# Kernel tuning notes

Measured on AMD Instinct MI355X. Metric: run time of the kernel, lower is better.

The kernel has to match this reference:

```python
import jax, jax.numpy as jnp
import numpy as np

N, E, D, L = 50000, 800000, 128, 4


def setup_inputs() -> dict:
    key = jax.random.key(0)
    k0, k1, k2, k3 = jax.random.split(key, 4)
    x = jax.random.normal(k0, (N, D), dtype=jnp.float32)
    edge_index = jax.random.randint(k1, (2, E), 0, N, dtype=jnp.int32)
    # per-layer GCNConv weights [L, D, D] and biases [L, D]
    W = jax.random.normal(k2, (L, D, D), dtype=jnp.float32) * (1.0 / np.sqrt(D))
    b = jax.random.normal(k3, (L, D), dtype=jnp.float32) * 0.01
    batch_index = jnp.zeros((N,), dtype=jnp.int32)
    node_rankings = jnp.zeros((N,), dtype=jnp.int32)
    return {"x": x, "edge_index": edge_index, "batch_index": batch_index,
            "node_rankings": node_rankings, "W": W, "b": b}


def reference(x, edge_index, batch_index, node_rankings, W, b):
    # NullControl contributes 0; dropout_rate=0 / eval -> identity.
    n = x.shape[0]
    loops = jnp.arange(n, dtype=edge_index.dtype)
    row = jnp.concatenate([edge_index[0], loops])  # sources (with self-loops)
    col = jnp.concatenate([edge_index[1], loops])  # destinations
    # symmetric GCN normalization: deg over destinations, norm = d_i^-1/2 d_j^-1/2
    deg = jax.ops.segment_sum(jnp.ones_like(row, dtype=x.dtype), col, num_segments=n)
    dinv = jnp.where(deg > 0, jax.lax.rsqrt(deg), 0.0)
    norm = dinv[row] * dinv[col]  # [E+N]
    for l in range(W.shape[0]):
        h = x @ W[l]                      # [N, D] dense transform
        msg = h[row] * norm[:, None]      # [E+N, D] gathered, scaled messages
        agg = jax.ops.segment_sum(msg, col, num_segments=n)  # scatter-add
        x = jax.nn.relu(agg + b[l])       # control(=0) + bias + relu
    return x
```

## Files before the change

kernel.cpp:

```cpp
#include <hip/hip_runtime.h>

#define D 128
#define NLAYERS 4

typedef unsigned short ushort_t;
typedef unsigned int uint_t;
typedef __attribute__((ext_vector_type(8))) short short8;
typedef __attribute__((ext_vector_type(4))) float f32x4;

__device__ __forceinline__ ushort_t f2bf(float f) {
    uint_t u = __float_as_uint(f);
    u += 0x7FFFu + ((u >> 16) & 1u);
    return (ushort_t)(u >> 16);
}
__device__ __forceinline__ float bf_lo(uint_t u) {
    return __uint_as_float(u << 16);
}
__device__ __forceinline__ float bf_hi(uint_t u) {
    return __uint_as_float(u & 0xFFFF0000u);
}
__device__ __forceinline__ uint_t pack2(float a, float b) {
    return (uint_t)f2bf(a) | ((uint_t)f2bf(b) << 16);
}


__global__ void k_count_deg(const int* __restrict__ dsts, int E,
                            int* __restrict__ deg, int* __restrict__ slot) {
    int i = blockIdx.x * blockDim.x + threadIdx.x;
    if (i < E) slot[i] = atomicAdd(&deg[dsts[i]], 1);
}

__global__ void k_scan1(const int* __restrict__ deg, int n, int* __restrict__ prow,
                        int* __restrict__ partials, float* __restrict__ dinv) {
    __shared__ int wsum[4];
    int tid = threadIdx.x;
    int base = blockIdx.x * 1024 + tid * 4;
    int g0 = (base + 0 < n) ? deg[base + 0] : -8;
    int g1 = (base + 1 < n) ? deg[base + 1] : -8;
    int g2 = (base + 2 < n) ? deg[base + 2] : -8;
    int g3 = (base + 3 < n) ? deg[base + 3] : -8;
    if (base + 0 < n) dinv[base + 0] = rsqrtf((float)(g0 + 1));
    if (base + 1 < n) dinv[base + 1] = rsqrtf((float)(g1 + 1));
    if (base + 2 < n) dinv[base + 2] = rsqrtf((float)(g2 + 1));
    if (base + 3 < n) dinv[base + 3] = rsqrtf((float)(g3 + 1));
    int p0 = (g0 + 8) & ~7;
    int p1 = (g1 + 8) & ~7;
    int p2 = (g2 + 8) & ~7;
    int p3 = (g3 + 8) & ~7;
    int s = p0 + p1 + p2 + p3;
    int lane = tid & 63;
    int incl = s;
    #pragma unroll
    for (int off = 1; off < 64; off <<= 1) {
        int y = __shfl_up(incl, off);
        if (lane >= off) incl += y;
    }
    int wid = tid >> 6;
    if (lane == 63) wsum[wid] = incl;
    __syncthreads();
    int wprev = 0;
    for (int w = 0; w < wid; w++) wprev += wsum[w];
    int excl = wprev + (incl - s);
    if (base + 0 < n) prow[base + 0] = excl;
    if (base + 1 < n) prow[base + 1] = excl + p0;
    if (base + 2 < n) prow[base + 2] = excl + p0 + p1;
    if (base + 3 < n) prow[base + 3] = excl + p0 + p1 + p2;
    if (tid == 255) partials[blockIdx.x] = wprev + incl;
}

__global__ void k_scan23(int* __restrict__ prow, const int* __restrict__ partials,
                         int n, int nb) {
    int i = blockIdx.x * blockDim.x + threadIdx.x;
    int chunk = (blockIdx.x * blockDim.x) >> 10;
    int pre = 0;
    for (int j = 0; j < chunk; j++) pre += partials[j];
    if (i < n) prow[i] += pre;
    if (i == 0) {
        int tot = 0;
        for (int j = 0; j < nb; j++) tot += partials[j];
        prow[n] = tot;
    }
}

__global__ void k_prep(const int* __restrict__ srcs, const int* __restrict__ dsts,
                       const int* __restrict__ deg, const int* __restrict__ slot,
                       const int* __restrict__ prow, const float* __restrict__ dinv,
                       const float* __restrict__ x, const float* __restrict__ W,
                       int* __restrict__ ewi, ushort_t* __restrict__ xs0,
                       ushort_t* __restrict__ xs1, ushort_t* __restrict__ Wt_hi,
                       ushort_t* __restrict__ Wt_lo, int n, int E,
                       int B1, int B2, int B3, int B4) {
    int b = blockIdx.x;
    int tid = threadIdx.x;
    if (b < B1) {
        int i = b * 256 + tid;
        if (i < E) {
            int c = dsts[i];
            ewi[prow[c] + 1 + slot[i]] = srcs[i];
        }
    } else if (b < B2) {
        int i = (b - B1) * 256 + tid;
        if (i < n) {
            int base = prow[i];
            int len = deg[i] + 1;
            int plen = (deg[i] + 8) & ~7;
            ewi[base] = i;
            for (int j = len; j < plen; j++) ewi[base + j] = n;
        }
    } else if (b < B3) {
        int idx = (b - B2) * 256 + tid;
        if (idx < n * (D / 4)) {
            int row = idx >> 5;
            float di = dinv[row];
            float4 v = ((const float4*)x)[idx];
            uint2 o;
            o.x = pack2(di * v.x, di * v.y);
            o.y = pack2(di * v.z, di * v.w);
            ((uint2*)xs0)[idx] = o;
        }
    } else if (b < B4) {
        int t = (b - B3) * 256 + tid;
        int l = t >> 14;
        int k = (t >> 7) & 127;
        int nn = t & 127;
        float w = W[((size_t)l << 14) + k * 128 + nn];
        ushort_t hi = f2bf(w);
        float wf = __uint_as_float((uint_t)hi << 16);
        ushort_t lo = f2bf(w - wf);
        size_t o = ((size_t)l << 14) + nn * 128 + k;
        Wt_hi[o] = hi;
        Wt_lo[o] = lo;
    } else {
        if (tid < 128) xs0[(size_t)n * D + tid] = 0;
        else xs1[(size_t)n * D + (tid - 128)] = 0;
    }
}

__global__ __launch_bounds__(256) void k_aggregate(
    const ushort_t* __restrict__ xs, const int* __restrict__ prow,
    const int* __restrict__ ewi, const float* __restrict__ dinv,
    ushort_t* __restrict__ s, int n) {
    int node = (blockIdx.x * 256 + threadIdx.x) >> 5;
    if (node >= n) return;
    int lane = threadIdx.x & 63;
    int sub = (lane >> 4) & 1;
    int t = lane & 15;
    float di = dinv[node];

    float acc[8] = {0.f, 0.f, 0.f, 0.f, 0.f, 0.f, 0.f, 0.f};
    int e = prow[node], end = prow[node + 1];
    for (; e < end; e += 8) {
        int4 gg = *(const int4*)(ewi + e + sub * 4);
        uint4 v0 = *(const uint4*)(xs + (size_t)gg.x * D + t * 8);
        uint4 v1 = *(const uint4*)(xs + (size_t)gg.y * D + t * 8);
        uint4 v2 = *(const uint4*)(xs + (size_t)gg.z * D + t * 8);
        uint4 v3 = *(const uint4*)(xs + (size_t)gg.w * D + t * 8);
        acc[0] += bf_lo(v0.x); acc[1] += bf_hi(v0.x);
        acc[2] += bf_lo(v0.y); acc[3] += bf_hi(v0.y);
        acc[4] += bf_lo(v0.z); acc[5] += bf_hi(v0.z);
        acc[6] += bf_lo(v0.w); acc[7] += bf_hi(v0.w);
        acc[0] += bf_lo(v1.x); acc[1] += bf_hi(v1.x);
        acc[2] += bf_lo(v1.y); acc[3] += bf_hi(v1.y);
        acc[4] += bf_lo(v1.z); acc[5] += bf_hi(v1.z);
        acc[6] += bf_lo(v1.w); acc[7] += bf_hi(v1.w);
        acc[0] += bf_lo(v2.x); acc[1] += bf_hi(v2.x);
        acc[2] += bf_lo(v2.y); acc[3] += bf_hi(v2.y);
        acc[4] += bf_lo(v2.z); acc[5] += bf_hi(v2.z);
        acc[6] += bf_lo(v2.w); acc[7] += bf_hi(v2.w);
        acc[0] += bf_lo(v3.x); acc[1] += bf_hi(v3.x);
        acc[2] += bf_lo(v3.y); acc[3] += bf_hi(v3.y);
        acc[4] += bf_lo(v3.z); acc[5] += bf_hi(v3.z);
        acc[6] += bf_lo(v3.w); acc[7] += bf_hi(v3.w);
    }
    #pragma unroll
    for (int q = 0; q < 8; q++) acc[q] += __shfl_xor(acc[q], 16);
    if (sub == 0) {
        ushort_t* dst = s + (size_t)node * D + t * 8;
        uint4 o;
        o.x = pack2(di * acc[0], di * acc[1]);
        o.y = pack2(di * acc[2], di * acc[3]);
        o.z = pack2(di * acc[4], di * acc[5]);
        o.w = pack2(di * acc[6], di * acc[7]);
        *(uint4*)dst = o;
    }
}

__global__ __launch_bounds__(256) void k_gemm_mfma(
    const ushort_t* __restrict__ A, const ushort_t* __restrict__ Wt_hi,
    const ushort_t* __restrict__ Wt_lo, const float* __restrict__ bias,
    const float* __restrict__ dinv, float* __restrict__ out_f32,
    ushort_t* __restrict__ out_bf, int n) {
    int tid = threadIdx.x;
    int wave = tid >> 6;
    int lane = tid & 63;
    int lg = lane >> 4;
    int lr = lane & 15;
    int base_row = blockIdx.x * 128 + wave * 32;

    short8 a[2][4];
    #pragma unroll
    for (int st = 0; st < 2; st++) {
        int r = base_row + st * 16 + lr;
        if (r > n - 1) r = n - 1;
        const ushort_t* ap = A + (size_t)r * D + lg * 8;
        #pragma unroll
        for (int k0 = 0; k0 < 4; k0++)
            a[st][k0] = *(const short8*)(ap + k0 * 32);
    }

    f32x4 acc[2][8];
    #pragma unroll
    for (int st = 0; st < 2; st++)
        #pragma unroll
        for (int nt = 0; nt < 8; nt++)
            acc[st][nt] = (f32x4){0.f, 0.f, 0.f, 0.f};

    #pragma unroll
    for (int nt = 0; nt < 8; nt++) {
        const ushort_t* wh = Wt_hi + (size_t)(nt * 16 + lr) * D + lg * 8;
        const ushort_t* wl = Wt_lo + (size_t)(nt * 16 + lr) * D + lg * 8;
        #pragma unroll
        for (int k0 = 0; k0 < 4; k0++) {
            short8 bh = *(const short8*)(wh + k0 * 32);
            short8 bl = *(const short8*)(wl + k0 * 32);
            acc[0][nt] = __builtin_amdgcn_mfma_f32_16x16x32_bf16(a[0][k0], bh, acc[0][nt], 0, 0, 0);
            acc[0][nt] = __builtin_amdgcn_mfma_f32_16x16x32_bf16(a[0][k0], bl, acc[0][nt], 0, 0, 0);
            acc[1][nt] = __builtin_amdgcn_mfma_f32_16x16x32_bf16(a[1][k0], bh, acc[1][nt], 0, 0, 0);
            acc[1][nt] = __builtin_amdgcn_mfma_f32_16x16x32_bf16(a[1][k0], bl, acc[1][nt], 0, 0, 0);
        }
    }

    #pragma unroll
    for (int nt = 0; nt < 8; nt++) {
        int col = nt * 16 + lr;
        float bv = bias[col];
        #pragma unroll
        for (int st = 0; st < 2; st++) {
            #pragma unroll
            for (int r = 0; r < 4; r++) {
                int grow = base_row + st * 16 + lg * 4 + r;
                float o = fmaxf(acc[st][nt][r] + bv, 0.f);
                float op = __shfl_xor(o, 1);
                if ((lr & 1) == 0 && grow < n) {
                    if (out_bf) {
                        float dsc = dinv[grow];
                        *(uint_t*)(out_bf + (size_t)grow * D + col) = pack2(dsc * o, dsc * op);
                    } else {
                        float2 ov; ov.x = o; ov.y = op;
                        *(float2*)(out_f32 + (size_t)grow * D + col) = ov;
                    }
                }
            }
        }
    }
}


extern "C" void kernel_launch(void* const* d_in, const int* in_sizes, int n_in,
                              void* d_out, int out_size, void* d_ws, size_t ws_size,
                              hipStream_t stream) {
    const float* x   = (const float*)d_in[0];
    const int* eidx  = (const int*)d_in[1];
    const float* W   = (const float*)d_in[4];
    const float* b   = (const float*)d_in[5];
    float* out       = (float*)d_out;

    const int N = in_sizes[0] / D;
    const int E = in_sizes[1] / 2;
    const int* srcs = eidx;
    const int* dsts = eidx + E;

    char* ws = (char*)d_ws;
    size_t off = 0;
    auto alloc = [&](size_t bytes) -> void* {
        void* p = ws + off;
        off = (off + bytes + 511) & ~(size_t)511;
        return p;
    };
    int*      deg      = (int*)alloc((size_t)N * 4);
    float*    dinv     = (float*)alloc((size_t)N * 4);
    int*      prow     = (int*)alloc((size_t)(N + 1) * 4);
    int*      partials = (int*)alloc(256 * 4);
    int*      ewi      = (int*)alloc((size_t)(E + 8 * N) * 4);
    ushort_t* s_buf    = (ushort_t*)alloc((size_t)N * D * 2);
    ushort_t* xh0      = (ushort_t*)alloc(((size_t)N + 1) * D * 2);
    ushort_t* xh1      = (ushort_t*)alloc(((size_t)N + 1) * D * 2);
    ushort_t* wt_hi    = (ushort_t*)alloc((size_t)NLAYERS * D * D * 2);
    ushort_t* wt_lo    = (ushort_t*)alloc((size_t)NLAYERS * D * D * 2);
    int*      slot     = (int*)s_buf;
    (void)ws_size; (void)n_in; (void)out_size;

    hipMemsetAsync(deg, 0, (size_t)N * 4, stream);

    int tE = (E + 255) / 256;
    int tN = (N + 255) / 256;
    int nbScan = (N + 1023) / 1024;

    k_count_deg<<<tE, 256, 0, stream>>>(dsts, E, deg, slot);
    k_scan1<<<nbScan, 256, 0, stream>>>(deg, N, prow, partials, dinv);
    k_scan23<<<tN, 256, 0, stream>>>(prow, partials, N, nbScan);

    int B1 = tE;
    int B2 = B1 + tN;
    int B3 = B2 + (N * (D / 4) + 255) / 256;
    int B4 = B3 + (NLAYERS * D * D) / 256;
    k_prep<<<B4 + 1, 256, 0, stream>>>(srcs, dsts, deg, slot, prow, dinv, x, W,
                                       ewi, xh0, xh1, wt_hi, wt_lo, N, E,
                                       B1, B2, B3, B4);

    int aggBlocks = (N + 7) / 8;
    int gemmBlocks = (N + 127) / 128;

    const ushort_t* xin = xh0;
    for (int l = 0; l < NLAYERS; l++) {
        k_aggregate<<<aggBlocks, 256, 0, stream>>>(xin, prow, ewi, dinv, s_buf, N);
        bool last = (l == NLAYERS - 1);
        ushort_t* xout = last ? nullptr : ((l & 1) ? xh0 : xh1);
        k_gemm_mfma<<<gemmBlocks, 256, 0, stream>>>(
            s_buf, wt_hi + (size_t)l * D * D, wt_lo + (size_t)l * D * D,
            b + (size_t)l * D, dinv, last ? out : nullptr, xout, N);
        xin = xout;
    }
}
```

Before: 372.8 us.

## Split bf16 feature matrices into 16-column panels for cache-local aggregation

```diff
diff --git a/kernel.cpp b/kernel.cpp
--- a/kernel.cpp
+++ b/kernel.cpp
@@ -2,6 +2,8 @@
 
 #define D 128
 #define NLAYERS 4
+#define NPANEL 8
+#define PCOLS 16
 
 typedef unsigned short ushort_t;
 typedef unsigned int uint_t;
@@ -90,6 +92,7 @@
                        ushort_t* __restrict__ xs1, ushort_t* __restrict__ Wt_hi,
                        ushort_t* __restrict__ Wt_lo, int n, int E,
                        int B1, int B2, int B3, int B4) {
+    const size_t PS = (size_t)(n + 1) * PCOLS;
     int b = blockIdx.x;
     int tid = threadIdx.x;
     if (b < B1) {
@@ -111,12 +114,13 @@
         int idx = (b - B2) * 256 + tid;
         if (idx < n * (D / 4)) {
             int row = idx >> 5;
+            int col0 = (idx & 31) * 4;
             float di = dinv[row];
             float4 v = ((const float4*)x)[idx];
             uint2 o;
             o.x = pack2(di * v.x, di * v.y);
             o.y = pack2(di * v.z, di * v.w);
-            ((uint2*)xs0)[idx] = o;
+            *(uint2*)(xs0 + (size_t)(col0 >> 4) * PS + (size_t)row * PCOLS + (col0 & 15)) = o;
         }
     } else if (b < B4) {
         int t = (b - B3) * 256 + tid;
@@ -131,8 +135,9 @@
         Wt_hi[o] = hi;
         Wt_lo[o] = lo;
     } else {
-        if (tid < 128) xs0[(size_t)n * D + tid] = 0;
-        else xs1[(size_t)n * D + (tid - 128)] = 0;
+        int q = (tid & 127) >> 4, w = tid & 15;
+        if (tid < 128) xs0[(size_t)q * PS + (size_t)n * PCOLS + w] = 0;
+        else           xs1[(size_t)q * PS + (size_t)n * PCOLS + w] = 0;
     }
 }
 
@@ -140,49 +145,37 @@
     const ushort_t* __restrict__ xs, const int* __restrict__ prow,
     const int* __restrict__ ewi, const float* __restrict__ dinv,
     ushort_t* __restrict__ s, int n) {
-    int node = (blockIdx.x * 256 + threadIdx.x) >> 5;
+    int node = (blockIdx.x * 256 + threadIdx.x) >> 3;
     if (node >= n) return;
-    int lane = threadIdx.x & 63;
-    int sub = (lane >> 4) & 1;
-    int t = lane & 15;
+    const size_t PS = (size_t)(n + 1) * PCOLS;
+    const ushort_t* xp = xs + (size_t)blockIdx.y * PS;
+    int c2 = (threadIdx.x & 7) * 2;
     float di = dinv[node];
 
-    float acc[8] = {0.f, 0.f, 0.f, 0.f, 0.f, 0.f, 0.f, 0.f};
+    float a0 = 0.f, a1 = 0.f;
     int e = prow[node], end = prow[node + 1];
     for (; e < end; e += 8) {
-        int4 gg = *(const int4*)(ewi + e + sub * 4);
-        uint4 v0 = *(const uint4*)(xs + (size_t)gg.x * D + t * 8);
-        uint4 v1 = *(const uint4*)(xs + (size_t)gg.y * D + t * 8);
-        uint4 v2 = *(const uint4*)(xs + (size_t)gg.z * D + t * 8);
-        uint4 v3 = *(const uint4*)(xs + (size_t)gg.w * D + t * 8);
-        acc[0] += bf_lo(v0.x); acc[1] += bf_hi(v0.x);
-        acc[2] += bf_lo(v0.y); acc[3] += bf_hi(v0.y);
-        acc[4] += bf_lo(v0.z); acc[5] += bf_hi(v0.z);
-        acc[6] += bf_lo(v0.w); acc[7] += bf_hi(v0.w);
-        acc[0] += bf_lo(v1.x); acc[1] += bf_hi(v1.x);
-        acc[2] += bf_lo(v1.y); acc[3] += bf_hi(v1.y);
-        acc[4] += bf_lo(v1.z); acc[5] += bf_hi(v1.z);
-        acc[6] += bf_lo(v1.w); acc[7] += bf_hi(v1.w);
-        acc[0] += bf_lo(v2.x); acc[1] += bf_hi(v2.x);
-        acc[2] += bf_lo(v2.y); acc[3] += bf_hi(v2.y);
-        acc[4] += bf_lo(v2.z); acc[5] += bf_hi(v2.z);
-        acc[6] += bf_lo(v2.w); acc[7] += bf_hi(v2.w);
-        acc[0] += bf_lo(v3.x); acc[1] += bf_hi(v3.x);
-        acc[2] += bf_lo(v3.y); acc[3] += bf_hi(v3.y);
-        acc[4] += bf_lo(v3.z); acc[5] += bf_hi(v3.z);
-        acc[6] += bf_lo(v3.w); acc[7] += bf_hi(v3.w);
-    }
-    #pragma unroll
-    for (int q = 0; q < 8; q++) acc[q] += __shfl_xor(acc[q], 16);
-    if (sub == 0) {
-        ushort_t* dst = s + (size_t)node * D + t * 8;
-        uint4 o;
-        o.x = pack2(di * acc[0], di * acc[1]);
-        o.y = pack2(di * acc[2], di * acc[3]);
-        o.z = pack2(di * acc[4], di * acc[5]);
-        o.w = pack2(di * acc[6], di * acc[7]);
-        *(uint4*)dst = o;
-    }
+        int4 sA = *(const int4*)(ewi + e);
+        int4 sB = *(const int4*)(ewi + e + 4);
+        uint_t v0 = *(const uint_t*)(xp + (size_t)sA.x * PCOLS + c2);
+        uint_t v1 = *(const uint_t*)(xp + (size_t)sA.y * PCOLS + c2);
+        uint_t v2 = *(const uint_t*)(xp + (size_t)sA.z * PCOLS + c2);
+        uint_t v3 = *(const uint_t*)(xp + (size_t)sA.w * PCOLS + c2);
+        uint_t v4 = *(const uint_t*)(xp + (size_t)sB.x * PCOLS + c2);
+        uint_t v5 = *(const uint_t*)(xp + (size_t)sB.y * PCOLS + c2);
+        uint_t v6 = *(const uint_t*)(xp + (size_t)sB.z * PCOLS + c2);
+        uint_t v7 = *(const uint_t*)(xp + (size_t)sB.w * PCOLS + c2);
+        a0 += bf_lo(v0); a1 += bf_hi(v0);
+        a0 += bf_lo(v1); a1 += bf_hi(v1);
+        a0 += bf_lo(v2); a1 += bf_hi(v2);
+        a0 += bf_lo(v3); a1 += bf_hi(v3);
+        a0 += bf_lo(v4); a1 += bf_hi(v4);
+        a0 += bf_lo(v5); a1 += bf_hi(v5);
+        a0 += bf_lo(v6); a1 += bf_hi(v6);
+        a0 += bf_lo(v7); a1 += bf_hi(v7);
+    }
+    *(uint_t*)(s + (size_t)blockIdx.y * PS + (size_t)node * PCOLS + c2) =
+        pack2(di * a0, di * a1);
 }
 
 __global__ __launch_bounds__(256) void k_gemm_mfma(
@@ -190,6 +183,7 @@
     const ushort_t* __restrict__ Wt_lo, const float* __restrict__ bias,
     const float* __restrict__ dinv, float* __restrict__ out_f32,
     ushort_t* __restrict__ out_bf, int n) {
+    const size_t PS = (size_t)(n + 1) * PCOLS;
     int tid = threadIdx.x;
     int wave = tid >> 6;
     int lane = tid & 63;
@@ -202,10 +196,11 @@
     for (int st = 0; st < 2; st++) {
         int r = base_row + st * 16 + lr;
         if (r > n - 1) r = n - 1;
-        const ushort_t* ap = A + (size_t)r * D + lg * 8;
         #pragma unroll
-        for (int k0 = 0; k0 < 4; k0++)
-            a[st][k0] = *(const short8*)(ap + k0 * 32);
+        for (int k0 = 0; k0 < 4; k0++) {
+            a[st][k0] = *(const short8*)(A + (size_t)((lg >> 1) + 2 * k0) * PS
+                                           + (size_t)r * PCOLS + (lg & 1) * 8);
+        }
     }
 
     f32x4 acc[2][8];
@@ -244,7 +239,8 @@
                 if ((lr & 1) == 0 && grow < n) {
                     if (out_bf) {
                         float dsc = dinv[grow];
-                        *(uint_t*)(out_bf + (size_t)grow * D + col) = pack2(dsc * o, dsc * op);
+                        *(uint_t*)(out_bf + (size_t)nt * PS + (size_t)grow * PCOLS + lr) =
+                            pack2(dsc * o, dsc * op);
                     } else {
                         float2 ov; ov.x = o; ov.y = op;
                         *(float2*)(out_f32 + (size_t)grow * D + col) = ov;
@@ -269,6 +265,8 @@
     const int E = in_sizes[1] / 2;
     const int* srcs = eidx;
     const int* dsts = eidx + E;
+
+    const size_t PS = (size_t)(N + 1) * PCOLS;
 
     char* ws = (char*)d_ws;
     size_t off = 0;
@@ -282,9 +280,9 @@
     int*      prow     = (int*)alloc((size_t)(N + 1) * 4);
     int*      partials = (int*)alloc(256 * 4);
     int*      ewi      = (int*)alloc((size_t)(E + 8 * N) * 4);
-    ushort_t* s_buf    = (ushort_t*)alloc((size_t)N * D * 2);
-    ushort_t* xh0      = (ushort_t*)alloc(((size_t)N + 1) * D * 2);
-    ushort_t* xh1      = (ushort_t*)alloc(((size_t)N + 1) * D * 2);
+    ushort_t* s_buf    = (ushort_t*)alloc(NPANEL * PS * 2);
+    ushort_t* xh0      = (ushort_t*)alloc(NPANEL * PS * 2);
+    ushort_t* xh1      = (ushort_t*)alloc(NPANEL * PS * 2);
     ushort_t* wt_hi    = (ushort_t*)alloc((size_t)NLAYERS * D * D * 2);
     ushort_t* wt_lo    = (ushort_t*)alloc((size_t)NLAYERS * D * D * 2);
     int*      slot     = (int*)s_buf;
@@ -308,12 +306,12 @@
                                        ewi, xh0, xh1, wt_hi, wt_lo, N, E,
                                        B1, B2, B3, B4);
 
-    int aggBlocks = (N + 7) / 8;
+    dim3 aggGrid((N + 31) / 32, NPANEL);
     int gemmBlocks = (N + 127) / 128;
 
     const ushort_t* xin = xh0;
     for (int l = 0; l < NLAYERS; l++) {
-        k_aggregate<<<aggBlocks, 256, 0, stream>>>(xin, prow, ewi, dinv, s_buf, N);
+        k_aggregate<<<aggGrid, 256, 0, stream>>>(xin, prow, ewi, dinv, s_buf, N);
         bool last = (l == NLAYERS - 1);
         ushort_t* xout = last ? nullptr : ((l & 1) ? xh0 : xh1);
         k_gemm_mfma<<<gemmBlocks, 256, 0, stream>>>(
```

New measurement: 424.0 us. +13.7%, slower.
